# Optimization experiments

Measured on AMD Instinct MI355X. Metric: run time of the kernel, lower is better.

## Reference

```python
import jax, jax.numpy as jnp
import numpy as np

N_NODES = 100000
N_EDGES = 1600000
D_IN = 256
D_OUT = 128


def _gcn_norm(edge_index, num_nodes):
    # Add self-loops and compute symmetric normalization D^-1/2 A D^-1/2 (PyG GCNConv default).
    src, dst = edge_index[0], edge_index[1]
    loop = jnp.arange(num_nodes, dtype=edge_index.dtype)
    src = jnp.concatenate([src, loop])
    dst = jnp.concatenate([dst, loop])
    deg = jax.ops.segment_sum(jnp.ones_like(dst, dtype=jnp.float32), dst, num_segments=num_nodes)
    dinv = jnp.where(deg > 0, jax.lax.rsqrt(jnp.maximum(deg, 1.0)), 0.0)
    norm = dinv[src] * dinv[dst]  # [E + N]
    return src, dst, norm


def _gcn_conv(x, W, b, src, dst, norm, num_nodes):
    h = x @ W  # [N, d_out] transform first (d_out <= d_in keeps message traffic low)
    msg = h[src] * norm[:, None]  # [E+N, d_out] gather + scale
    out = jax.ops.segment_sum(msg, dst, num_segments=num_nodes)  # scatter-add
    return out + b


def setup_inputs() -> dict:
    key = jax.random.key(0)
    ks = jax.random.split(key, 8)
    x = jax.random.normal(ks[0], (N_NODES, D_IN), dtype=jnp.float32)
    edge_index = jax.random.randint(ks[1], (2, N_EDGES), 0, N_NODES, dtype=jnp.int64)
    s = 0.05
    return {
        "x": x,
        "edge_index": edge_index,
        "W1": jax.random.normal(ks[2], (D_IN, D_OUT), dtype=jnp.float32) * s,
        "b1": jnp.zeros((D_OUT,), dtype=jnp.float32),
        "W_mu": jax.random.normal(ks[3], (D_OUT, D_OUT), dtype=jnp.float32) * s,
        "b_mu": jnp.zeros((D_OUT,), dtype=jnp.float32),
        "W_ls": jax.random.normal(ks[4], (D_OUT, D_OUT), dtype=jnp.float32) * s,
        "b_ls": jnp.zeros((D_OUT,), dtype=jnp.float32),
    }


def reference(x, edge_index, W1, b1, W_mu, b_mu, W_ls, b_ls):
    num_nodes = x.shape[0]
    src, dst, norm = _gcn_norm(edge_index, num_nodes)
    h = jax.nn.relu(_gcn_conv(x, W1, b1, src, dst, norm, num_nodes))
    mu = _gcn_conv(h, W_mu, b_mu, src, dst, norm, num_nodes)
    logstd = _gcn_conv(h, W_ls, b_ls, src, dst, norm, num_nodes)
    return (mu, logstd)
```

## Files before the change

kernel.cpp:

```cpp
#include <hip/hip_runtime.h>
#include <hip/hip_bf16.h>
#include <hip/hip_fp16.h>

typedef __attribute__((ext_vector_type(8))) short short8;
typedef __attribute__((ext_vector_type(8))) _Float16 f16x8;
typedef __attribute__((ext_vector_type(4))) float f32x4;

#define EPB 16384

__global__ __launch_bounds__(256) void k_lhist(const int* __restrict__ dst, int* __restrict__ histT,
                                               int nE, int nblk, int nbins) {
  __shared__ int c[1024];
  int tid = threadIdx.x;
  for (int i = tid; i < nbins; i += 256) c[i] = 0;
  __syncthreads();
  int blk = blockIdx.x;
  int e0 = blk * EPB;
  int e1 = min(nE, e0 + EPB);
  if (e1 - e0 == EPB) {
#pragma unroll
    for (int it = 0; it < EPB / 1024; ++it) {
      int4 d = *(const int4*)(dst + e0 + it * 1024 + tid * 4);
      atomicAdd(&c[d.x >> 7], 1);
      atomicAdd(&c[d.y >> 7], 1);
      atomicAdd(&c[d.z >> 7], 1);
      atomicAdd(&c[d.w >> 7], 1);
    }
  } else {
    for (int i = e0 + tid; i < e1; i += 256) atomicAdd(&c[dst[i] >> 7], 1);
  }
  __syncthreads();
  for (int i = tid; i < nbins; i += 256) histT[i * nblk + blk] = c[i];
}

__global__ __launch_bounds__(256) void k_lscatter(
    const int* __restrict__ src, const int* __restrict__ dst, const int* __restrict__ subPtr,
    int* __restrict__ binned, int nE, int nblk, int nbins) {
  __shared__ int cur[1024];
  int tid = threadIdx.x;
  int blk = blockIdx.x;
  for (int i = tid; i < nbins; i += 256) cur[i] = subPtr[i * nblk + blk];
  __syncthreads();
  int e0 = blk * EPB;
  int e1 = min(nE, e0 + EPB);
  if (e1 - e0 == EPB) {
#pragma unroll
    for (int it = 0; it < EPB / 1024; ++it) {
      int base = e0 + it * 1024 + tid * 4;
      int4 s = *(const int4*)(src + base);
      int4 d = *(const int4*)(dst + base);
      int p0 = atomicAdd(&cur[d.x >> 7], 1);
      int p1 = atomicAdd(&cur[d.y >> 7], 1);
      int p2 = atomicAdd(&cur[d.z >> 7], 1);
      int p3 = atomicAdd(&cur[d.w >> 7], 1);
      binned[p0] = s.x | ((d.x & 127) << 20);
      binned[p1] = s.y | ((d.y & 127) << 20);
      binned[p2] = s.z | ((d.z & 127) << 20);
      binned[p3] = s.w | ((d.w & 127) << 20);
    }
  } else {
    for (int i = e0 + tid; i < e1; i += 256) {
      int d = dst[i];
      int pos = atomicAdd(&cur[d >> 7], 1);
      binned[pos] = src[i] | ((d & 127) << 20);
    }
  }
}

__global__ __launch_bounds__(256) void k_bin_cnt(
    const int* __restrict__ binned, const int* __restrict__ subPtr,
    int* __restrict__ cnt, int nE, int nblk, int nbins, int n) {
  __shared__ int c128[128];
  int b = blockIdx.x;
  int tid = threadIdx.x;
  if (tid < 128) c128[tid] = 0;
  __syncthreads();
  int s0 = subPtr[b * nblk];
  int s1 = (b + 1 < nbins) ? subPtr[(b + 1) * nblk] : nE;
  for (int i = s0 + tid; i < s1; i += 256)
    atomicAdd(&c128[(binned[i] >> 20) & 127], 1);
  __syncthreads();
  if (tid < 128) {
    int idx = (b << 7) + tid;
    if (idx < n) cnt[idx] = c128[tid];
  }
}

__global__ __launch_bounds__(256) void k_bin_place(
    const int* __restrict__ binned, const int* __restrict__ subPtr,
    const int* __restrict__ rowptr, int* __restrict__ col, int nE, int nblk, int nbins, int n) {
  __shared__ int cur128[128];
  int b = blockIdx.x;
  int tid = threadIdx.x;
  if (tid < 128) {
    int idx = (b << 7) + tid;
    cur128[tid] = (idx < n) ? rowptr[idx] : 0;
  }
  __syncthreads();
  int s0 = subPtr[b * nblk];
  int s1 = (b + 1 < nbins) ? subPtr[(b + 1) * nblk] : nE;
  for (int i = s0 + tid; i < s1; i += 256) {
    int e = binned[i];
    int pos = atomicAdd(&cur128[(e >> 20) & 127], 1);
    col[pos] = e & 0xFFFFF;
  }
}


__global__ void k_blocksum(const int* __restrict__ cnt, int* __restrict__ bsum, int n) {
  __shared__ int red[256];
  int tid = threadIdx.x;
  int base = blockIdx.x * 1024 + tid * 4;
  int s = 0;
#pragma unroll
  for (int i = 0; i < 4; i++) { int idx = base + i; if (idx < n) s += cnt[idx]; }
  red[tid] = s;
  __syncthreads();
  for (int off = 128; off > 0; off >>= 1) {
    if (tid < off) red[tid] += red[tid + off];
    __syncthreads();
  }
  if (tid == 0) bsum[blockIdx.x] = red[0];
}

__global__ void k_scan_bsum(int* __restrict__ bsum, int nb) {
  __shared__ int s[128];
  int tid = threadIdx.x;
  int v = (tid < nb) ? bsum[tid] : 0;
  s[tid] = v;
  __syncthreads();
  for (int off = 1; off < 128; off <<= 1) {
    int t = (tid >= off) ? s[tid - off] : 0;
    __syncthreads();
    s[tid] += t;
    __syncthreads();
  }
  if (tid < nb) bsum[tid] = s[tid] - v;
}

__global__ void k_scan_final(const int* __restrict__ cnt, const int* __restrict__ bsum,
                             int* __restrict__ rowptr, float* __restrict__ dinv, int n) {
  __shared__ int tsum[256];
  int tid = threadIdx.x;
  int base = blockIdx.x * 1024 + tid * 4;
  int v[4]; int s = 0;
#pragma unroll
  for (int i = 0; i < 4; i++) { v[i] = (base + i < n) ? cnt[base + i] : 0; s += v[i]; }
  tsum[tid] = s;
  __syncthreads();
  for (int off = 1; off < 256; off <<= 1) {
    int t = (tid >= off) ? tsum[tid - off] : 0;
    __syncthreads();
    tsum[tid] += t;
    __syncthreads();
  }
  int run = bsum[blockIdx.x] + tsum[tid] - s;
#pragma unroll
  for (int i = 0; i < 4; i++) {
    int idx = base + i;
    if (idx < n) {
      rowptr[idx] = run;
      if (dinv) dinv[idx] = rsqrtf((float)(v[i] + 1));
      run += v[i];
    }
  }
}


__global__ void k_prep_w(const float* __restrict__ W1,
                         const float* __restrict__ Wmu, const float* __restrict__ Wls,
                         const float* __restrict__ bmu, const float* __restrict__ bls,
                         __half* __restrict__ W1T, __half* __restrict__ WcT,
                         float* __restrict__ bcat) {
  int i = blockIdx.x * blockDim.x + threadIdx.x;
  if (i < 128 * 256) {
    int n = i >> 8, k = i & 255;
    W1T[i] = __float2half(W1[k * 128 + n]);
  } else if (i < 2 * 128 * 256) {
    int j = i - 128 * 256;
    int n = j >> 7, k = j & 127;
    float f = (n < 128) ? Wmu[k * 128 + n] : Wls[k * 128 + (n - 128)];
    WcT[j] = __float2half(f);
  } else if (i < 2 * 128 * 256 + 256) {
    int n = i - 2 * 128 * 256;
    bcat[n] = (n < 128) ? bmu[n] : bls[n - 128];
  }
}


#define LP 40

__global__ __launch_bounds__(256) void k_gemm_mfma(
    const float* __restrict__ Av, const __half* __restrict__ WT,
    __half* __restrict__ out0, int M, int K) {
  __shared__ _Float16 As[128 * LP];
  __shared__ _Float16 Bs[128 * LP];

  const int tid = threadIdx.x;
  const int lane = tid & 63;
  const int wv = tid >> 6;
  const int wr = wv >> 1, wc = wv & 1;
  const int rsel = lane >> 4;
  const int rrow = lane & 15;
  const int row0 = blockIdx.x * 128;
  const int col0 = 0;

  f32x4 acc[4][4];
#pragma unroll
  for (int m = 0; m < 4; m++)
#pragma unroll
    for (int n = 0; n < 4; n++) acc[m][n] = (f32x4){0.f, 0.f, 0.f, 0.f};

  const int srow = tid >> 1;
  const int skh = (tid & 1) * 16;

  for (int k0 = 0; k0 < K; k0 += 32) {
    if (row0 + srow < M) {
      const float* src = Av + (size_t)(row0 + srow) * K + k0 + skh;
      float4 f0 = *(const float4*)(src);
      float4 f1 = *(const float4*)(src + 4);
      float4 f2 = *(const float4*)(src + 8);
      float4 f3 = *(const float4*)(src + 12);
      f16x8 v0, v1;
      v0[0]=(_Float16)f0.x; v0[1]=(_Float16)f0.y; v0[2]=(_Float16)f0.z; v0[3]=(_Float16)f0.w;
      v0[4]=(_Float16)f1.x; v0[5]=(_Float16)f1.y; v0[6]=(_Float16)f1.z; v0[7]=(_Float16)f1.w;
      v1[0]=(_Float16)f2.x; v1[1]=(_Float16)f2.y; v1[2]=(_Float16)f2.z; v1[3]=(_Float16)f2.w;
      v1[4]=(_Float16)f3.x; v1[5]=(_Float16)f3.y; v1[6]=(_Float16)f3.z; v1[7]=(_Float16)f3.w;
      *(f16x8*)&As[srow * LP + skh]     = v0;
      *(f16x8*)&As[srow * LP + skh + 8] = v1;
    } else {
      f16x8 z = (f16x8){0,0,0,0,0,0,0,0};
      *(f16x8*)&As[srow * LP + skh] = z; *(f16x8*)&As[srow * LP + skh + 8] = z;
    }
    {
      const _Float16* s = (const _Float16*)WT + (size_t)(col0 + srow) * K + k0 + skh;
      *(f16x8*)&Bs[srow * LP + skh]     = *(const f16x8*)s;
      *(f16x8*)&Bs[srow * LP + skh + 8] = *(const f16x8*)(s + 8);
    }
    __syncthreads();

    f16x8 fa[4], fb[4];
#pragma unroll
    for (int m = 0; m < 4; m++)
      fa[m] = *(f16x8*)&As[(wr * 64 + m * 16 + rrow) * LP + rsel * 8];
#pragma unroll
    for (int n = 0; n < 4; n++)
      fb[n] = *(f16x8*)&Bs[(wc * 64 + n * 16 + rrow) * LP + rsel * 8];
#pragma unroll
    for (int m = 0; m < 4; m++)
#pragma unroll
      for (int n = 0; n < 4; n++)
        acc[m][n] = __builtin_amdgcn_mfma_f32_16x16x32_f16(fa[m], fb[n], acc[m][n], 0, 0, 0);
    __syncthreads();
  }

#pragma unroll
  for (int n = 0; n < 4; n++) {
    int c = col0 + wc * 64 + n * 16 + rrow;
#pragma unroll
    for (int m = 0; m < 4; m++) {
      f32x4 v = acc[m][n];
#pragma unroll
      for (int r = 0; r < 4; r++) {
        int row = row0 + wr * 64 + m * 16 + rsel * 4 + r;
        if (row < M) out0[(size_t)row * 128 + c] = __float2half(v[r]);
      }
    }
  }
}


__global__ __launch_bounds__(256) void k_spmm_h(
    const __half* __restrict__ in, const int* __restrict__ rowptr,
    const int* __restrict__ cnt, const int* __restrict__ col,
    const float* __restrict__ dinv,
    const float* __restrict__ bias, __half* __restrict__ out,
    int n, int use_bias, int relu_out) {
  int node = blockIdx.x * 4 + (threadIdx.x >> 6);
  if (node >= n) return;
  int lane = threadIdx.x & 63;

  const __half2* inp = (const __half2*)in;
  float di = dinv[node];
  float2 v = __half22float2(inp[(size_t)node * 64 + lane]);
  float accx = di * v.x;
  float accy = di * v.y;

  int beg = rowptr[node];
  int m = cnt[node];
  int i = 0;
  for (; i + 8 <= m; i += 8) {
    int c[8];
#pragma unroll
    for (int j = 0; j < 8; j++) c[j] = col[beg + i + j];
    float e[8];
#pragma unroll
    for (int j = 0; j < 8; j++) e[j] = dinv[c[j]];
    float2 u[8];
#pragma unroll
    for (int j = 0; j < 8; j++) u[j] = __half22float2(inp[(size_t)c[j] * 64 + lane]);
#pragma unroll
    for (int j = 0; j < 8; j++) { accx += e[j] * u[j].x; accy += e[j] * u[j].y; }
  }
  if (i < m) {
    int c[8];
#pragma unroll
    for (int j = 0; j < 8; j++) c[j] = col[(i + j < m) ? (beg + i + j) : beg];
    float e[8];
#pragma unroll
    for (int j = 0; j < 8; j++) e[j] = (i + j < m) ? dinv[c[j]] : 0.f;
    float2 u[8];
#pragma unroll
    for (int j = 0; j < 8; j++) u[j] = __half22float2(inp[(size_t)c[j] * 64 + lane]);
#pragma unroll
    for (int j = 0; j < 8; j++) { accx += e[j] * u[j].x; accy += e[j] * u[j].y; }
  }
  accx *= di;
  accy *= di;
  if (use_bias) {
    accx += bias[2 * lane];
    accy += bias[2 * lane + 1];
  }
  if (relu_out) {
    accx = fmaxf(accx, 0.f);
    accy = fmaxf(accy, 0.f);
  }
  ((__half2*)(out + (size_t)node * 128))[lane] = __floats2half2_rn(accx, accy);
}


__global__ __launch_bounds__(512) void k_spmm_gemm(
    const __half* __restrict__ in, const int* __restrict__ rowptr,
    const int* __restrict__ cnt, const int* __restrict__ col,
    const float* __restrict__ dinv,
    const __half* __restrict__ WcT, const float* __restrict__ bcat,
    float* __restrict__ out0, float* __restrict__ out1, int n) {
  __shared__ _Float16 gt[16 * 128];
  const int tid = threadIdx.x;
  const int lane = tid & 63;
  const int w = tid >> 6;
  const __half2* inp = (const __half2*)in;

#pragma unroll
  for (int q = 0; q < 2; q++) {
    int li = w * 2 + q;
    int node = blockIdx.x * 16 + li;
    float accx = 0.f, accy = 0.f;
    if (node < n) {
      float di = dinv[node];
      float2 v = __half22float2(inp[(size_t)node * 64 + lane]);
      accx = di * v.x;
      accy = di * v.y;
      int beg = rowptr[node];
      int m = cnt[node];
      int i = 0;
      for (; i + 8 <= m; i += 8) {
        int c[8];
#pragma unroll
        for (int j = 0; j < 8; j++) c[j] = col[beg + i + j];
        float e[8];
#pragma unroll
        for (int j = 0; j < 8; j++) e[j] = dinv[c[j]];
        float2 u[8];
#pragma unroll
        for (int j = 0; j < 8; j++) u[j] = __half22float2(inp[(size_t)c[j] * 64 + lane]);
#pragma unroll
        for (int j = 0; j < 8; j++) { accx += e[j] * u[j].x; accy += e[j] * u[j].y; }
      }
      if (i < m) {
        int c[8];
#pragma unroll
        for (int j = 0; j < 8; j++) c[j] = col[(i + j < m) ? (beg + i + j) : beg];
        float e[8];
#pragma unroll
        for (int j = 0; j < 8; j++) e[j] = (i + j < m) ? dinv[c[j]] : 0.f;
        float2 u[8];
#pragma unroll
        for (int j = 0; j < 8; j++) u[j] = __half22float2(inp[(size_t)c[j] * 64 + lane]);
#pragma unroll
        for (int j = 0; j < 8; j++) { accx += e[j] * u[j].x; accy += e[j] * u[j].y; }
      }
      accx *= di;
      accy *= di;
    }
    int slot = (lane >> 2) ^ (li & 7);
    *(__half2*)((char*)gt + li * 256 + slot * 16 + (lane & 3) * 4) =
        __floats2half2_rn(accx, accy);
  }
  __syncthreads();

  const int lr = lane & 15;
  const int lk = lane >> 4;
  f16x8 a[4];
#pragma unroll
  for (int ks = 0; ks < 4; ks++) {
    int slot = (ks * 4 + lk) ^ (lr & 7);
    a[ks] = *(const f16x8*)((const char*)gt + lr * 256 + slot * 16);
  }
#pragma unroll
  for (int ct = 0; ct < 2; ct++) {
    int colg = (w * 2 + ct) * 16 + lr;
    f32x4 acc = (f32x4){0.f, 0.f, 0.f, 0.f};
#pragma unroll
    for (int ks = 0; ks < 4; ks++) {
      f16x8 b = *(const f16x8*)((const _Float16*)WcT + (size_t)colg * 128 + ks * 32 + lk * 8);
      acc = __builtin_amdgcn_mfma_f32_16x16x32_f16(a[ks], b, acc, 0, 0, 0);
    }
    float badd = bcat[colg];
    float* dst = out0;
    int c = colg;
    if (c >= 128) { dst = out1; c -= 128; }
#pragma unroll
    for (int r = 0; r < 4; r++) {
      int node = blockIdx.x * 16 + lk * 4 + r;
      if (node < n) dst[(size_t)node * 128 + c] = acc[r] + badd;
    }
  }
}


extern "C" void kernel_launch(void* const* d_in, const int* in_sizes, int n_in,
                              void* d_out, int out_size, void* d_ws, size_t ws_size,
                              hipStream_t stream) {
  const float* x   = (const float*)d_in[0];
  const int*   ei  = (const int*)d_in[1];
  const float* W1  = (const float*)d_in[2];
  const float* b1  = (const float*)d_in[3];
  const float* Wmu = (const float*)d_in[4];
  const float* bmu = (const float*)d_in[5];
  const float* Wls = (const float*)d_in[6];
  const float* bls = (const float*)d_in[7];

  int N = in_sizes[0] / 256;
  int E = in_sizes[1] / 2;
  const int* src = ei;
  const int* dst = ei + E;

  int NBINS = (N + 127) >> 7;
  int NBLK  = (E + EPB - 1) / EPB;
  int NS    = NBINS * NBLK;

  char* ws = (char*)d_ws;
  size_t o = 0;
  auto alloc = [&](size_t b) { size_t c = o; o = (o + b + 511) & ~(size_t)511; return c; };
  int*   cnt     = (int*)(ws + alloc((size_t)N * 4));
  int*   rowptr  = (int*)(ws + alloc((size_t)N * 4));
  float* dinv    = (float*)(ws + alloc((size_t)N * 4));
  int*   bsum    = (int*)(ws + alloc(512));
  int*   histT   = (int*)(ws + alloc((size_t)NS * 4));
  int*   subPtr  = (int*)(ws + alloc((size_t)NS * 4));
  int*   col     = (int*)(ws + alloc((size_t)E * 4));
  int*   binned  = (int*)(ws + alloc((size_t)E * 4));
  __half* W1T  = (__half*)(ws + alloc(128 * 256 * 2));
  __half* WcT  = (__half*)(ws + alloc(256 * 128 * 2));
  float*  bcat = (float*)(ws + alloc(256 * 4));
  __half* h0   = (__half*)(ws + alloc((size_t)N * 128 * 2));
  __half* hBuf = (__half*)(ws + alloc((size_t)N * 128 * 2));

  float* outMu = (float*)d_out;
  float* outLs = outMu + (size_t)N * 128;

  int nbScanN = (N + 1023) / 1024;
  int nbScanS = (NS + 1023) / 1024;

  k_lhist<<<NBLK, 256, 0, stream>>>(dst, histT, E, NBLK, NBINS);
  k_blocksum<<<nbScanS, 256, 0, stream>>>(histT, bsum, NS);
  k_scan_bsum<<<1, 128, 0, stream>>>(bsum, nbScanS);
  k_scan_final<<<nbScanS, 256, 0, stream>>>(histT, bsum, subPtr, nullptr, NS);
  k_lscatter<<<NBLK, 256, 0, stream>>>(src, dst, subPtr, binned, E, NBLK, NBINS);
  k_bin_cnt<<<NBINS, 256, 0, stream>>>(binned, subPtr, cnt, E, NBLK, NBINS, N);
  k_blocksum<<<nbScanN, 256, 0, stream>>>(cnt, bsum, N);
  k_scan_bsum<<<1, 128, 0, stream>>>(bsum, nbScanN);
  k_scan_final<<<nbScanN, 256, 0, stream>>>(cnt, bsum, rowptr, dinv, N);
  k_bin_place<<<NBINS, 256, 0, stream>>>(binned, subPtr, rowptr, col, E, NBLK, NBINS, N);

  k_prep_w<<<(2 * 128 * 256 + 256 + 255) / 256, 256, 0, stream>>>(
      W1, Wmu, Wls, bmu, bls, W1T, WcT, bcat);

  k_gemm_mfma<<<(N + 127) / 128, 256, 0, stream>>>(x, W1T, h0, N, 256);
  k_spmm_h<<<(N + 3) / 4, 256, 0, stream>>>(h0, rowptr, cnt, col, dinv, b1, hBuf, N, 1, 1);
  k_spmm_gemm<<<(N + 15) / 16, 512, 0, stream>>>(
      hBuf, rowptr, cnt, col, dinv, WcT, bcat, outMu, outLs, N);
}
```

Measured before the change: 300.6 us.

## Fuse bin count, row-pointer scan and placement; shrink spmm_gemm blocks

The per-bin count, the global node-degree scan and the column placement are merged into a single k_bin_finish kernel. Each bin already knows its edge offset from subPtr, so row pointers come from a local 128-entry scan in shared memory, and the three global scan launches and one extra pass over binned are removed. Separately, k_spmm_gemm now runs with 256 threads per block, with each wave handling 4 nodes and 4 column tiles instead of 2. That trades per-block parallelism for fewer waves per block and may change occupancy.

```diff
diff --git a/kernel.cpp b/kernel.cpp
--- a/kernel.cpp
+++ b/kernel.cpp
@@ -67,10 +67,14 @@
   }
 }
 
-__global__ __launch_bounds__(256) void k_bin_cnt(
+
+__global__ __launch_bounds__(256) void k_bin_finish(
     const int* __restrict__ binned, const int* __restrict__ subPtr,
-    int* __restrict__ cnt, int nE, int nblk, int nbins, int n) {
+    int* __restrict__ cnt, int* __restrict__ rowptr, float* __restrict__ dinv,
+    int* __restrict__ col, int nE, int nblk, int nbins, int n) {
   __shared__ int c128[128];
+  __shared__ int scan128[128];
+  __shared__ int cur128[128];
   int b = blockIdx.x;
   int tid = threadIdx.x;
   if (tid < 128) c128[tid] = 0;
@@ -80,25 +84,28 @@
   for (int i = s0 + tid; i < s1; i += 256)
     atomicAdd(&c128[(binned[i] >> 20) & 127], 1);
   __syncthreads();
+  if (tid < 128) scan128[tid] = c128[tid];
+  __syncthreads();
+  for (int off = 1; off < 128; off <<= 1) {
+    int t = 0;
+    if (tid < 128 && tid >= off) t = scan128[tid - off];
+    __syncthreads();
+    if (tid < 128) scan128[tid] += t;
+    __syncthreads();
+  }
   if (tid < 128) {
+    int v = c128[tid];
+    int excl = scan128[tid] - v;
+    int rp = s0 + excl;
     int idx = (b << 7) + tid;
-    if (idx < n) cnt[idx] = c128[tid];
-  }
-}
-
-__global__ __launch_bounds__(256) void k_bin_place(
-    const int* __restrict__ binned, const int* __restrict__ subPtr,
-    const int* __restrict__ rowptr, int* __restrict__ col, int nE, int nblk, int nbins, int n) {
-  __shared__ int cur128[128];
-  int b = blockIdx.x;
-  int tid = threadIdx.x;
-  if (tid < 128) {
-    int idx = (b << 7) + tid;
-    cur128[tid] = (idx < n) ? rowptr[idx] : 0;
-  }
-  __syncthreads();
-  int s0 = subPtr[b * nblk];
-  int s1 = (b + 1 < nbins) ? subPtr[(b + 1) * nblk] : nE;
+    if (idx < n) {
+      cnt[idx] = v;
+      rowptr[idx] = rp;
+      dinv[idx] = rsqrtf((float)(v + 1));
+    }
+    cur128[tid] = rp;
+  }
+  __syncthreads();
   for (int i = s0 + tid; i < s1; i += 256) {
     int e = binned[i];
     int pos = atomicAdd(&cur128[(e >> 20) & 127], 1);
@@ -139,7 +146,7 @@
 }
 
 __global__ void k_scan_final(const int* __restrict__ cnt, const int* __restrict__ bsum,
-                             int* __restrict__ rowptr, float* __restrict__ dinv, int n) {
+                             int* __restrict__ rowptr, int n) {
   __shared__ int tsum[256];
   int tid = threadIdx.x;
   int base = blockIdx.x * 1024 + tid * 4;
@@ -158,11 +165,7 @@
 #pragma unroll
   for (int i = 0; i < 4; i++) {
     int idx = base + i;
-    if (idx < n) {
-      rowptr[idx] = run;
-      if (dinv) dinv[idx] = rsqrtf((float)(v[i] + 1));
-      run += v[i];
-    }
+    if (idx < n) { rowptr[idx] = run; run += v[i]; }
   }
 }
 
@@ -203,7 +206,6 @@
   const int rsel = lane >> 4;
   const int rrow = lane & 15;
   const int row0 = blockIdx.x * 128;
-  const int col0 = 0;
 
   f32x4 acc[4][4];
 #pragma unroll
@@ -233,7 +235,7 @@
       *(f16x8*)&As[srow * LP + skh] = z; *(f16x8*)&As[srow * LP + skh + 8] = z;
     }
     {
-      const _Float16* s = (const _Float16*)WT + (size_t)(col0 + srow) * K + k0 + skh;
+      const _Float16* s = (const _Float16*)WT + (size_t)srow * K + k0 + skh;
       *(f16x8*)&Bs[srow * LP + skh]     = *(const f16x8*)s;
       *(f16x8*)&Bs[srow * LP + skh + 8] = *(const f16x8*)(s + 8);
     }
@@ -256,7 +258,7 @@
 
 #pragma unroll
   for (int n = 0; n < 4; n++) {
-    int c = col0 + wc * 64 + n * 16 + rrow;
+    int c = wc * 64 + n * 16 + rrow;
 #pragma unroll
     for (int m = 0; m < 4; m++) {
       f32x4 v = acc[m][n];
@@ -329,7 +331,7 @@
 }
 
 
-__global__ __launch_bounds__(512) void k_spmm_gemm(
+__global__ __launch_bounds__(256) void k_spmm_gemm(
     const __half* __restrict__ in, const int* __restrict__ rowptr,
     const int* __restrict__ cnt, const int* __restrict__ col,
     const float* __restrict__ dinv,
@@ -341,9 +343,8 @@
   const int w = tid >> 6;
   const __half2* inp = (const __half2*)in;
 
-#pragma unroll
-  for (int q = 0; q < 2; q++) {
-    int li = w * 2 + q;
+  for (int q = 0; q < 4; q++) {
+    int li = w * 4 + q;
     int node = blockIdx.x * 16 + li;
     float accx = 0.f, accy = 0.f;
     if (node < n) {
@@ -398,8 +399,8 @@
     a[ks] = *(const f16x8*)((const char*)gt + lr * 256 + slot * 16);
   }
 #pragma unroll
-  for (int ct = 0; ct < 2; ct++) {
-    int colg = (w * 2 + ct) * 16 + lr;
+  for (int ct = 0; ct < 4; ct++) {
+    int colg = (w * 4 + ct) * 16 + lr;
     f32x4 acc = (f32x4){0.f, 0.f, 0.f, 0.f};
 #pragma unroll
     for (int ks = 0; ks < 4; ks++) {
@@ -460,25 +461,21 @@
   float* outMu = (float*)d_out;
   float* outLs = outMu + (size_t)N * 128;
 
-  int nbScanN = (N + 1023) / 1024;
   int nbScanS = (NS + 1023) / 1024;
 
   k_lhist<<<NBLK, 256, 0, stream>>>(dst, histT, E, NBLK, NBINS);
   k_blocksum<<<nbScanS, 256, 0, stream>>>(histT, bsum, NS);
   k_scan_bsum<<<1, 128, 0, stream>>>(bsum, nbScanS);
-  k_scan_final<<<nbScanS, 256, 0, stream>>>(histT, bsum, subPtr, nullptr, NS);
+  k_scan_final<<<nbScanS, 256, 0, stream>>>(histT, bsum, subPtr, NS);
   k_lscatter<<<NBLK, 256, 0, stream>>>(src, dst, subPtr, binned, E, NBLK, NBINS);
-  k_bin_cnt<<<NBINS, 256, 0, stream>>>(binned, subPtr, cnt, E, NBLK, NBINS, N);
-  k_blocksum<<<nbScanN, 256, 0, stream>>>(cnt, bsum, N);
-  k_scan_bsum<<<1, 128, 0, stream>>>(bsum, nbScanN);
-  k_scan_final<<<nbScanN, 256, 0, stream>>>(cnt, bsum, rowptr, dinv, N);
-  k_bin_place<<<NBINS, 256, 0, stream>>>(binned, subPtr, rowptr, col, E, NBLK, NBINS, N);
+  k_bin_finish<<<NBINS, 256, 0, stream>>>(binned, subPtr, cnt, rowptr, dinv, col,
+                                          E, NBLK, NBINS, N);
 
   k_prep_w<<<(2 * 128 * 256 + 256 + 255) / 256, 256, 0, stream>>>(
       W1, Wmu, Wls, bmu, bls, W1T, WcT, bcat);
 
   k_gemm_mfma<<<(N + 127) / 128, 256, 0, stream>>>(x, W1T, h0, N, 256);
   k_spmm_h<<<(N + 3) / 4, 256, 0, stream>>>(h0, rowptr, cnt, col, dinv, b1, hBuf, N, 1, 1);
-  k_spmm_gemm<<<(N + 15) / 16, 512, 0, stream>>>(
+  k_spmm_gemm<<<(N + 15) / 16, 256, 0, stream>>>(
       hBuf, rowptr, cnt, col, dinv, WcT, bcat, outMu, outLs, N);
 }
```

Measured after the change: 289.9 us. 1.04x faster.
